# Kernel optimization log

Measured on AMD Instinct MI355X. Metric: run time of the kernel, lower is better.

Reference implementation:

```python
import jax, jax.numpy as jnp
import numpy as np

N = 268  # nodes per graph (4288 / nhid=16)


def _cheb_norm(edge_index, edge_weight):
    # PyG ChebConv normalization with normalization='sym', lambda_max=2.0:
    # L_hat = (2/lambda_max) * L - I = -D^{-1/2} A D^{-1/2} (diagonal cancels to 0)
    row, col = edge_index[0], edge_index[1]
    deg = jax.ops.segment_sum(edge_weight, row, num_segments=N)
    dis = jnp.where(deg > 0, jax.lax.rsqrt(deg), 0.0)
    return -edge_weight * dis[row] * dis[col]


def _cheb_conv(x, edge_index, norm, w, b):
    # K=2: out = T0 @ W0 + T1 @ W1 + b,  T0 = x, T1 = L_hat x
    row, col = edge_index[0], edge_index[1]
    tx1 = jax.ops.segment_sum(norm[:, None] * x[col], row, num_segments=N)
    return x @ w[0] + tx1 @ w[1] + b


def _forward_single(x, edge_index, edge_attr, gc1_w, gc1_b, gc4_w, gc4_b):
    norm = _cheb_norm(edge_index, edge_attr)
    h = jax.nn.relu(_cheb_conv(x, edge_index, norm, gc1_w, gc1_b))
    # dropout in eval mode -> identity
    return _cheb_conv(h, edge_index, norm, gc4_w, gc4_b)  # [N, nhid]


def setup_inputs() -> dict:
    key = jax.random.key(0)
    ks = jax.random.split(key, 20)
    B, E, F, H = 64, 8576, 268, 16
    inp = {}
    for i, nm in enumerate(['x1', 'x2', 'x3']):
        inp[nm] = jax.random.normal(ks[i], (B, N, F), dtype=jnp.float32)
    for i, nm in enumerate(['edge_index1', 'edge_index2', 'edge_index3']):
        inp[nm] = jax.random.randint(ks[3 + i], (B, 2, E), 0, N)
    for i, nm in enumerate(['edge_attr1', 'edge_attr2', 'edge_attr3']):
        inp[nm] = jax.random.uniform(ks[6 + i], (B, E), dtype=jnp.float32)
    s = 0.05
    inp['gc1_w'] = jax.random.normal(ks[9], (2, F, H), dtype=jnp.float32) * s
    inp['gc1_b'] = jnp.zeros((H,), dtype=jnp.float32)
    inp['gc4_w'] = jax.random.normal(ks[10], (2, H, H), dtype=jnp.float32) * s
    inp['gc4_b'] = jnp.zeros((H,), dtype=jnp.float32)
    inp['fc1_w'] = jax.random.normal(ks[11], (1024, N * H), dtype=jnp.float32) * s
    inp['fc1_b'] = jnp.zeros((1024,), dtype=jnp.float32)
    inp['fc2_w'] = jax.random.normal(ks[12], (512, 1024), dtype=jnp.float32) * s
    inp['fc2_b'] = jnp.zeros((512,), dtype=jnp.float32)
    return inp


def reference(x1, x2, x3, edge_index1, edge_index2, edge_index3,
              edge_attr1, edge_attr2, edge_attr3,
              gc1_w, gc1_b, gc4_w, gc4_b, fc1_w, fc1_b, fc2_w, fc2_b):
    conv = jax.vmap(_forward_single, in_axes=(0, 0, 0, None, None, None, None))

    def branch(x, ei, ea):
        c = conv(x, ei, ea, gc1_w, gc1_b, gc4_w, gc4_b)      # [B, N, H]
        f = c.reshape(c.shape[0], -1)                        # [B, 4288]
        h = jax.nn.relu(f @ fc1_w.T + fc1_b)                 # classifier dropout: eval -> id
        return h @ fc2_w.T + fc2_b                           # [B, 512]

    return (branch(x1, edge_index1, edge_attr1),
            branch(x2, edge_index2, edge_attr2),
            branch(x3, edge_index3, edge_attr3))
```

## Files before the change

kernel.cpp:

```cpp
#include <hip/hip_runtime.h>


#define NN   268
#define EE   8576
#define NG   192
#define FDIM 4288
#define CONVT 1024

typedef __bf16 bf16_t;
typedef bf16_t bf16x8 __attribute__((ext_vector_type(8)));
typedef bf16_t bf16x4 __attribute__((ext_vector_type(4)));
typedef float  f32x4  __attribute__((ext_vector_type(4)));

#define XW0_OFF  0
#define XW1_OFF  (XW0_OFF + (size_t)NG * FDIM)
#define WB_OFF   (XW1_OFF + (size_t)NG * FDIM)
#define FB_OFF   (WB_OFF + 2195456)
#define WXT_OFF  (FB_OFF + 411648)
#define H1_OFF   (WXT_OFF + 4608)
#define R1P_OFF  (H1_OFF + 196608)
#define R2P_OFF  (R1P_OFF + 1572864)

#define NCASTB 2144

__global__ __launch_bounds__(256) void k_prep(
    const float* __restrict__ fc1w, const float* __restrict__ gc1w,
    bf16_t* __restrict__ wb, bf16_t* __restrict__ wxt)
{
    if (blockIdx.x < NCASTB) {
        const size_t base = ((size_t)blockIdx.x * 256 + threadIdx.x) * 8;
        const float4 a = *(const float4*)(fc1w + base);
        const float4 b = *(const float4*)(fc1w + base + 4);
        bf16x8 v;
        v[0] = (bf16_t)a.x; v[1] = (bf16_t)a.y; v[2] = (bf16_t)a.z; v[3] = (bf16_t)a.w;
        v[4] = (bf16_t)b.x; v[5] = (bf16_t)b.y; v[6] = (bf16_t)b.z; v[7] = (bf16_t)b.w;
        *(bf16x8*)(wb + base) = v;
    } else {
        for (int idx = threadIdx.x; idx < 2 * 9 * 64; idx += 256) {
            const int lane = idx & 63, chunk = (idx >> 6) % 9, nt = idx / (9 * 64);
            const int n = lane & 15, q = lane >> 4;
            bf16x8 v;
#pragma unroll
            for (int j = 0; j < 8; ++j) {
                const int k = chunk * 32 + q * 8 + j;
                v[j] = (k < NN) ? (bf16_t)gc1w[nt * FDIM + k * 16 + n] : (bf16_t)0.f;
            }
            *(bf16x8*)(wxt + (size_t)idx * 8) = v;
        }
    }
}

__global__ __launch_bounds__(64) void k_xw(
    const float* __restrict__ x0, const float* __restrict__ x1, const float* __restrict__ x2,
    const bf16_t* __restrict__ wxt, float* __restrict__ xw0, float* __restrict__ xw1)
{
    const int g = blockIdx.y;
    const int br = g >> 6, b = g & 63;
    const float* x = ((br == 0) ? x0 : (br == 1) ? x1 : x2) + (size_t)b * (NN * NN);
    const int lane = threadIdx.x;
    const int q = lane >> 4, nlo = lane & 15;
    const int mrow = blockIdx.x * 16 + nlo;
    const bool mvalid = (mrow < NN);
    const float* xrow = x + (size_t)mrow * NN;

    f32x4 acc0 = {0.f, 0.f, 0.f, 0.f}, acc1 = {0.f, 0.f, 0.f, 0.f};
    for (int ch = 0; ch < 9; ++ch) {
        const int k0 = ch * 32 + q * 8;
        float4 p0 = make_float4(0.f, 0.f, 0.f, 0.f);
        float4 p1 = make_float4(0.f, 0.f, 0.f, 0.f);
        if (mvalid) {
            if (k0 < NN)     p0 = *(const float4*)(xrow + k0);
            if (k0 + 4 < NN) p1 = *(const float4*)(xrow + k0 + 4);
        }
        bf16x8 a;
        a[0] = (bf16_t)p0.x; a[1] = (bf16_t)p0.y; a[2] = (bf16_t)p0.z; a[3] = (bf16_t)p0.w;
        a[4] = (bf16_t)p1.x; a[5] = (bf16_t)p1.y; a[6] = (bf16_t)p1.z; a[7] = (bf16_t)p1.w;
        const bf16x8 b0 = *(const bf16x8*)(wxt + (size_t)(ch * 64 + lane) * 8);
        const bf16x8 b1 = *(const bf16x8*)(wxt + (size_t)(576 + ch * 64 + lane) * 8);
        acc0 = __builtin_amdgcn_mfma_f32_16x16x32_bf16(a, b0, acc0, 0, 0, 0);
        acc1 = __builtin_amdgcn_mfma_f32_16x16x32_bf16(a, b1, acc1, 0, 0, 0);
    }
    const int col = nlo;
#pragma unroll
    for (int r = 0; r < 4; ++r) {
        const int row = blockIdx.x * 16 + q * 4 + r;
        if (row < NN) {
            xw0[((size_t)g * NN + row) * 16 + col] = acc0[r];
            xw1[((size_t)g * NN + row) * 16 + col] = acc1[r];
        }
    }
}

__global__ __launch_bounds__(CONVT) void k_conv(
    const int* __restrict__ ei0, const int* __restrict__ ei1, const int* __restrict__ ei2,
    const float* __restrict__ ea0, const float* __restrict__ ea1, const float* __restrict__ ea2,
    const float* __restrict__ xw0, const float* __restrict__ xw1,
    const float* __restrict__ gc1b, const float* __restrict__ gc4w,
    const float* __restrict__ gc4b, bf16_t* __restrict__ fout)
{
    const int g = blockIdx.x;
    const int br = g >> 6, b = g & 63;
    const int*   ei = (br == 0) ? ei0 : (br == 1) ? ei1 : ei2;
    const float* ea = (br == 0) ? ea0 : (br == 1) ? ea1 : ea2;
    const int*   rowp = ei + (size_t)b * (2 * EE);
    const int*   colp = rowp + EE;
    const float* eap  = ea + (size_t)b * EE;

    __shared__ unsigned int e_s[EE];
    __shared__ __align__(16) bf16_t A_s[FDIM];
    __shared__ __align__(16) bf16_t S_s[FDIM];
    __shared__ float degS[NN];
    __shared__ int   cntS[NN];
    __shared__ int   offS[NN + 1];
    __shared__ int   curS[NN];
    __shared__ float w4_s[512];
    __shared__ float b1_s[16];
    __shared__ float b4_s[16];
    const int tid = threadIdx.x;

    if (tid < NN) { degS[tid] = 0.f; cntS[tid] = 0; }
    if (tid < 512) w4_s[tid] = gc4w[tid];
    if (tid < 16) { b1_s[tid] = gc1b[tid]; b4_s[tid] = gc4b[tid]; }
    {
        const float4* src = (const float4*)(xw1 + (size_t)g * FDIM);
        for (int i = tid; i < FDIM / 4; i += CONVT) {
            const float4 v = src[i];
            bf16x4 o; o[0] = (bf16_t)v.x; o[1] = (bf16_t)v.y; o[2] = (bf16_t)v.z; o[3] = (bf16_t)v.w;
            *(bf16x4*)&A_s[i * 4] = o;
        }
    }
    __syncthreads();
    for (int e = tid; e < EE; e += CONVT) {
        const int r = rowp[e];
        atomicAdd(&degS[r], eap[e]);
        atomicAdd(&cntS[r], 1);
    }
    for (int st = 1; st < NN; st <<= 1) {
        __syncthreads();
        int v = 0;
        if (tid < NN) { v = cntS[tid]; if (tid >= st) v += cntS[tid - st]; }
        __syncthreads();
        if (tid < NN) cntS[tid] = v;
    }
    __syncthreads();
    if (tid < NN) offS[tid + 1] = cntS[tid];
    if (tid == 0) offS[0] = 0;
    __syncthreads();
    if (tid < NN) {
        curS[tid] = offS[tid];
        const float d = degS[tid];
        degS[tid] = (d > 0.f) ? rsqrtf(d) : 0.f;
    }
    __syncthreads();
    for (int e = tid; e < EE; e += CONVT) {
        const int r = rowp[e], c = colp[e];
        const float nv = -eap[e] * degS[r] * degS[c];
        union { float f; unsigned u; } cv; cv.f = nv;
        const unsigned bits = (cv.u + 0x7fffu + ((cv.u >> 16) & 1u)) >> 16;
        const int pos = atomicAdd(&curS[r], 1);
        e_s[pos] = ((unsigned)c << 16) | bits;
    }
    __syncthreads();

    const int j4 = tid & 3, nl = tid >> 2;
    const bf16x4* A4 = (const bf16x4*)A_s;
    const float4* xw0g = (const float4*)(xw0 + (size_t)g * FDIM);

    for (int n = nl; n < NN; n += 256) {
        const int s = offS[n], e = offS[n + 1];
        float ax = 0.f, ay = 0.f, az = 0.f, aw = 0.f;
        int i = s;
        for (; i + 3 < e; i += 4) {
            const unsigned p0 = e_s[i], p1 = e_s[i + 1], p2 = e_s[i + 2], p3 = e_s[i + 3];
            const float w0 = __uint_as_float(p0 << 16);
            const float w1 = __uint_as_float(p1 << 16);
            const float w2 = __uint_as_float(p2 << 16);
            const float w3 = __uint_as_float(p3 << 16);
            const bf16x4 a0 = A4[(p0 >> 16) * 4 + j4];
            const bf16x4 a1 = A4[(p1 >> 16) * 4 + j4];
            const bf16x4 a2 = A4[(p2 >> 16) * 4 + j4];
            const bf16x4 a3 = A4[(p3 >> 16) * 4 + j4];
            ax += w0 * (float)a0[0] + w1 * (float)a1[0] + w2 * (float)a2[0] + w3 * (float)a3[0];
            ay += w0 * (float)a0[1] + w1 * (float)a1[1] + w2 * (float)a2[1] + w3 * (float)a3[1];
            az += w0 * (float)a0[2] + w1 * (float)a1[2] + w2 * (float)a2[2] + w3 * (float)a3[2];
            aw += w0 * (float)a0[3] + w1 * (float)a1[3] + w2 * (float)a2[3] + w3 * (float)a3[3];
        }
        for (; i < e; ++i) {
            const unsigned p0 = e_s[i];
            const float w0 = __uint_as_float(p0 << 16);
            const bf16x4 a0 = A4[(p0 >> 16) * 4 + j4];
            ax += w0 * (float)a0[0]; ay += w0 * (float)a0[1];
            az += w0 * (float)a0[2]; aw += w0 * (float)a0[3];
        }
        const float4 xv = xw0g[n * 4 + j4];
        bf16x4 h;
        h[0] = (bf16_t)fmaxf(xv.x + ax + b1_s[j4 * 4 + 0], 0.f);
        h[1] = (bf16_t)fmaxf(xv.y + ay + b1_s[j4 * 4 + 1], 0.f);
        h[2] = (bf16_t)fmaxf(xv.z + az + b1_s[j4 * 4 + 2], 0.f);
        h[3] = (bf16_t)fmaxf(xv.w + aw + b1_s[j4 * 4 + 3], 0.f);
        *(bf16x4*)&S_s[n * 16 + j4 * 4] = h;
    }
    __syncthreads();

    for (int idx = tid; idx < FDIM; idx += CONVT) {
        const int n = idx >> 4, j = idx & 15;
        const bf16x8 s0 = *(const bf16x8*)&S_s[n * 16];
        const bf16x8 s1 = *(const bf16x8*)&S_s[n * 16 + 8];
        float a1 = 0.f;
#pragma unroll
        for (int k = 0; k < 8; ++k) a1 += (float)s0[k] * w4_s[256 + k * 16 + j];
#pragma unroll
        for (int k = 0; k < 8; ++k) a1 += (float)s1[k] * w4_s[256 + (k + 8) * 16 + j];
        A_s[idx] = (bf16_t)a1;
    }
    __syncthreads();

    for (int n = nl; n < NN; n += 256) {
        const int s = offS[n], e = offS[n + 1];
        float ax = 0.f, ay = 0.f, az = 0.f, aw = 0.f;
        int i = s;
        for (; i + 3 < e; i += 4) {
            const unsigned p0 = e_s[i], p1 = e_s[i + 1], p2 = e_s[i + 2], p3 = e_s[i + 3];
            const float w0 = __uint_as_float(p0 << 16);
            const float w1 = __uint_as_float(p1 << 16);
            const float w2 = __uint_as_float(p2 << 16);
            const float w3 = __uint_as_float(p3 << 16);
            const bf16x4 a0 = A4[(p0 >> 16) * 4 + j4];
            const bf16x4 a1 = A4[(p1 >> 16) * 4 + j4];
            const bf16x4 a2 = A4[(p2 >> 16) * 4 + j4];
            const bf16x4 a3 = A4[(p3 >> 16) * 4 + j4];
            ax += w0 * (float)a0[0] + w1 * (float)a1[0] + w2 * (float)a2[0] + w3 * (float)a3[0];
            ay += w0 * (float)a0[1] + w1 * (float)a1[1] + w2 * (float)a2[1] + w3 * (float)a3[1];
            az += w0 * (float)a0[2] + w1 * (float)a1[2] + w2 * (float)a2[2] + w3 * (float)a3[2];
            aw += w0 * (float)a0[3] + w1 * (float)a1[3] + w2 * (float)a2[3] + w3 * (float)a3[3];
        }
        for (; i < e; ++i) {
            const unsigned p0 = e_s[i];
            const float w0 = __uint_as_float(p0 << 16);
            const bf16x4 a0 = A4[(p0 >> 16) * 4 + j4];
            ax += w0 * (float)a0[0]; ay += w0 * (float)a0[1];
            az += w0 * (float)a0[2]; aw += w0 * (float)a0[3];
        }
        float h0[4];
#pragma unroll
        for (int c2 = 0; c2 < 4; ++c2) h0[c2] = b4_s[j4 * 4 + c2];
        const bf16x8 s0 = *(const bf16x8*)&S_s[n * 16];
        const bf16x8 s1 = *(const bf16x8*)&S_s[n * 16 + 8];
#pragma unroll
        for (int k = 0; k < 8; ++k) {
            const float sv = (float)s0[k];
#pragma unroll
            for (int c2 = 0; c2 < 4; ++c2) h0[c2] += sv * w4_s[k * 16 + j4 * 4 + c2];
        }
#pragma unroll
        for (int k = 0; k < 8; ++k) {
            const float sv = (float)s1[k];
#pragma unroll
            for (int c2 = 0; c2 < 4; ++c2) h0[c2] += sv * w4_s[(k + 8) * 16 + j4 * 4 + c2];
        }
        bf16x4 o;
        o[0] = (bf16_t)(h0[0] + ax); o[1] = (bf16_t)(h0[1] + ay);
        o[2] = (bf16_t)(h0[2] + az); o[3] = (bf16_t)(h0[3] + aw);
        *(bf16x4*)(fout + (size_t)g * FDIM + n * 16 + j4 * 4) = o;
    }
}

__global__ __launch_bounds__(256) void k_fc1(
    const bf16_t* __restrict__ fb, const bf16_t* __restrict__ wb, float* __restrict__ r1p)
{
    const int mt = blockIdx.x, nb = blockIdx.y, kz = blockIdx.z;
    const int wid = threadIdx.x >> 6, lane = threadIdx.x & 63;
    const int q = lane >> 4, nlo = lane & 15;
    const int n0 = nb * 128 + wid * 32;
    const int cstart = kz * 17;
    const int ccnt   = (kz == 7) ? 15 : 17;

    const bf16_t* arow = fb + (size_t)(mt * 16 + nlo) * FDIM + q * 8;
    const bf16_t* brow = wb + (size_t)(n0 + nlo) * FDIM + q * 8;
    f32x4 acc[2];
#pragma unroll
    for (int t = 0; t < 2; ++t) { acc[t][0]=0.f; acc[t][1]=0.f; acc[t][2]=0.f; acc[t][3]=0.f; }

    for (int ch = 0; ch < ccnt; ++ch) {
        const size_t ko = (size_t)(cstart + ch) * 32;
        const bf16x8 a = *(const bf16x8*)(arow + ko);
#pragma unroll
        for (int t = 0; t < 2; ++t) {
            const bf16x8 bv = *(const bf16x8*)(brow + (size_t)t * 16 * FDIM + ko);
            acc[t] = __builtin_amdgcn_mfma_f32_16x16x32_bf16(a, bv, acc[t], 0, 0, 0);
        }
    }
    float* outp = r1p + (size_t)kz * (NG * 1024);
#pragma unroll
    for (int t = 0; t < 2; ++t)
#pragma unroll
        for (int r = 0; r < 4; ++r)
            outp[(size_t)(mt * 16 + q * 4 + r) * 1024 + n0 + t * 16 + nlo] = acc[t][r];
}

__global__ __launch_bounds__(256) void k_red1(
    const float* __restrict__ r1p, const float* __restrict__ b1, float* __restrict__ h1)
{
    const size_t i = ((size_t)blockIdx.x * 256 + threadIdx.x) * 4;
    const size_t S = (size_t)NG * 1024;
    float4 s = *(const float4*)(r1p + i);
#pragma unroll
    for (int k = 1; k < 8; ++k) {
        const float4 t = *(const float4*)(r1p + (size_t)k * S + i);
        s.x += t.x; s.y += t.y; s.z += t.z; s.w += t.w;
    }
    const float4 bb = *(const float4*)(b1 + (i & 1023));
    float4 o;
    o.x = fmaxf(s.x + bb.x, 0.f);
    o.y = fmaxf(s.y + bb.y, 0.f);
    o.z = fmaxf(s.z + bb.z, 0.f);
    o.w = fmaxf(s.w + bb.w, 0.f);
    *(float4*)(h1 + i) = o;
}

__global__ __launch_bounds__(256) void k_fc2(
    const float* __restrict__ h1, const float* __restrict__ w2, float* __restrict__ r2p)
{
    const int m0 = blockIdx.x * 64;
    const int n0 = blockIdx.y * 64;
    const int kb = blockIdx.z * 64;
    __shared__ float rs[64][68];
    __shared__ float wss[64][68];
    const int tid = threadIdx.x;
    const int mt = tid & 15, nt = tid >> 4;
    float acc[4][4];
#pragma unroll
    for (int i = 0; i < 4; ++i)
#pragma unroll
        for (int j = 0; j < 4; ++j) acc[i][j] = 0.f;

    for (int idx = tid; idx < 1024; idx += 256) {
        const int r = idx >> 4, qq = idx & 15;
        const int gk = kb + qq * 4;
        *(float4*)&rs[r][qq * 4]  = *(const float4*)(h1 + (size_t)(m0 + r) * 1024 + gk);
        *(float4*)&wss[r][qq * 4] = *(const float4*)(w2 + (size_t)(n0 + r) * 1024 + gk);
    }
    __syncthreads();
    for (int kq = 0; kq < 16; ++kq) {
        float4 av[4], bv[4];
#pragma unroll
        for (int i = 0; i < 4; ++i) av[i] = *(const float4*)&rs[mt + 16 * i][kq * 4];
#pragma unroll
        for (int j = 0; j < 4; ++j) bv[j] = *(const float4*)&wss[nt + 16 * j][kq * 4];
#pragma unroll
        for (int i = 0; i < 4; ++i)
#pragma unroll
            for (int j = 0; j < 4; ++j)
                acc[i][j] += av[i].x * bv[j].x + av[i].y * bv[j].y +
                             av[i].z * bv[j].z + av[i].w * bv[j].w;
    }
    float* outp = r2p + (size_t)blockIdx.z * (NG * 512);
#pragma unroll
    for (int i = 0; i < 4; ++i)
#pragma unroll
        for (int j = 0; j < 4; ++j)
            outp[(size_t)(m0 + mt + 16 * i) * 512 + n0 + nt + 16 * j] = acc[i][j];
}

__global__ __launch_bounds__(256) void k_red2(
    const float* __restrict__ r2p, const float* __restrict__ b2, float* __restrict__ out)
{
    const size_t i = ((size_t)blockIdx.x * 256 + threadIdx.x) * 4;
    const size_t S = (size_t)NG * 512;
    float4 s = *(const float4*)(r2p + i);
#pragma unroll
    for (int k = 1; k < 16; ++k) {
        const float4 t = *(const float4*)(r2p + (size_t)k * S + i);
        s.x += t.x; s.y += t.y; s.z += t.z; s.w += t.w;
    }
    const float4 bb = *(const float4*)(b2 + (i & 511));
    s.x += bb.x; s.y += bb.y; s.z += bb.z; s.w += bb.w;
    *(float4*)(out + i) = s;
}

extern "C" void kernel_launch(void* const* d_in, const int* in_sizes, int n_in,
                              void* d_out, int out_size, void* d_ws, size_t ws_size,
                              hipStream_t stream)
{
    const float* x0   = (const float*)d_in[0];
    const float* x1   = (const float*)d_in[1];
    const float* x2   = (const float*)d_in[2];
    const int*   ei0  = (const int*)d_in[3];
    const int*   ei1  = (const int*)d_in[4];
    const int*   ei2  = (const int*)d_in[5];
    const float* ea0  = (const float*)d_in[6];
    const float* ea1  = (const float*)d_in[7];
    const float* ea2  = (const float*)d_in[8];
    const float* gc1w = (const float*)d_in[9];
    const float* gc1b = (const float*)d_in[10];
    const float* gc4w = (const float*)d_in[11];
    const float* gc4b = (const float*)d_in[12];
    const float* fc1w = (const float*)d_in[13];
    const float* fc1b = (const float*)d_in[14];
    const float* fc2w = (const float*)d_in[15];
    const float* fc2b = (const float*)d_in[16];

    float*  ws  = (float*)d_ws;
    float*  xw0 = ws + XW0_OFF;
    float*  xw1 = ws + XW1_OFF;
    bf16_t* wb  = (bf16_t*)(ws + WB_OFF);
    bf16_t* fb  = (bf16_t*)(ws + FB_OFF);
    bf16_t* wxt = (bf16_t*)(ws + WXT_OFF);
    float*  h1  = ws + H1_OFF;
    float*  r1p = ws + R1P_OFF;
    float*  r2p = ws + R2P_OFF;
    float*  out = (float*)d_out;

    k_prep<<<NCASTB + 1, 256, 0, stream>>>(fc1w, gc1w, wb, wxt);
    k_xw  <<<dim3(17, NG), 64, 0, stream>>>(x0, x1, x2, wxt, xw0, xw1);
    k_conv<<<NG, CONVT, 0, stream>>>(ei0, ei1, ei2, ea0, ea1, ea2,
                                     xw0, xw1, gc1b, gc4w, gc4b, fb);
    k_fc1 <<<dim3(12, 8, 8), 256, 0, stream>>>(fb, wb, r1p);
    k_red1<<<NG, 256, 0, stream>>>(r1p, fc1b, h1);
    k_fc2 <<<dim3(3, 8, 16), 256, 0, stream>>>(h1, fc2w, r2p);
    k_red2<<<96, 256, 0, stream>>>(r2p, fc2b, out);
}
```

Measured before the change: 225.2 us.

## Fuse x@W0/W1 MFMA projection into conv kernel, keep results in LDS

Removes the separate k_xw kernel and computes the x·gc1_w projections inside k_conv, with 16 waves each handling a 16-row tile via bf16 MFMA. The results go straight into shared memory (xw0 as float, xw1 as bf16 in A_s), so the global round trip of the xw buffers and one kernel launch disappear. In exchange the x projection now runs on only 192 blocks instead of 17×192 small blocks. Each wave's MFMA loop is serialized (17 tiles on 16 waves, so one wave does two), and the extra LDS array may lower occupancy.

```diff
diff --git a/kernel.cpp b/kernel.cpp
--- a/kernel.cpp
+++ b/kernel.cpp
@@ -12,10 +12,8 @@
 typedef bf16_t bf16x4 __attribute__((ext_vector_type(4)));
 typedef float  f32x4  __attribute__((ext_vector_type(4)));
 
-#define XW0_OFF  0
-#define XW1_OFF  (XW0_OFF + (size_t)NG * FDIM)
-#define WB_OFF   (XW1_OFF + (size_t)NG * FDIM)
-#define FB_OFF   (WB_OFF + 2195456)
+#define WB_OFF   0
+#define FB_OFF   2195456
 #define WXT_OFF  (FB_OFF + 411648)
 #define H1_OFF   (WXT_OFF + 4608)
 #define R1P_OFF  (H1_OFF + 196608)
@@ -50,56 +48,17 @@
     }
 }
 
-__global__ __launch_bounds__(64) void k_xw(
+__global__ __launch_bounds__(CONVT) void k_conv(
     const float* __restrict__ x0, const float* __restrict__ x1, const float* __restrict__ x2,
-    const bf16_t* __restrict__ wxt, float* __restrict__ xw0, float* __restrict__ xw1)
-{
-    const int g = blockIdx.y;
-    const int br = g >> 6, b = g & 63;
-    const float* x = ((br == 0) ? x0 : (br == 1) ? x1 : x2) + (size_t)b * (NN * NN);
-    const int lane = threadIdx.x;
-    const int q = lane >> 4, nlo = lane & 15;
-    const int mrow = blockIdx.x * 16 + nlo;
-    const bool mvalid = (mrow < NN);
-    const float* xrow = x + (size_t)mrow * NN;
-
-    f32x4 acc0 = {0.f, 0.f, 0.f, 0.f}, acc1 = {0.f, 0.f, 0.f, 0.f};
-    for (int ch = 0; ch < 9; ++ch) {
-        const int k0 = ch * 32 + q * 8;
-        float4 p0 = make_float4(0.f, 0.f, 0.f, 0.f);
-        float4 p1 = make_float4(0.f, 0.f, 0.f, 0.f);
-        if (mvalid) {
-            if (k0 < NN)     p0 = *(const float4*)(xrow + k0);
-            if (k0 + 4 < NN) p1 = *(const float4*)(xrow + k0 + 4);
-        }
-        bf16x8 a;
-        a[0] = (bf16_t)p0.x; a[1] = (bf16_t)p0.y; a[2] = (bf16_t)p0.z; a[3] = (bf16_t)p0.w;
-        a[4] = (bf16_t)p1.x; a[5] = (bf16_t)p1.y; a[6] = (bf16_t)p1.z; a[7] = (bf16_t)p1.w;
-        const bf16x8 b0 = *(const bf16x8*)(wxt + (size_t)(ch * 64 + lane) * 8);
-        const bf16x8 b1 = *(const bf16x8*)(wxt + (size_t)(576 + ch * 64 + lane) * 8);
-        acc0 = __builtin_amdgcn_mfma_f32_16x16x32_bf16(a, b0, acc0, 0, 0, 0);
-        acc1 = __builtin_amdgcn_mfma_f32_16x16x32_bf16(a, b1, acc1, 0, 0, 0);
-    }
-    const int col = nlo;
-#pragma unroll
-    for (int r = 0; r < 4; ++r) {
-        const int row = blockIdx.x * 16 + q * 4 + r;
-        if (row < NN) {
-            xw0[((size_t)g * NN + row) * 16 + col] = acc0[r];
-            xw1[((size_t)g * NN + row) * 16 + col] = acc1[r];
-        }
-    }
-}
-
-__global__ __launch_bounds__(CONVT) void k_conv(
     const int* __restrict__ ei0, const int* __restrict__ ei1, const int* __restrict__ ei2,
     const float* __restrict__ ea0, const float* __restrict__ ea1, const float* __restrict__ ea2,
-    const float* __restrict__ xw0, const float* __restrict__ xw1,
+    const bf16_t* __restrict__ wxt,
     const float* __restrict__ gc1b, const float* __restrict__ gc4w,
     const float* __restrict__ gc4b, bf16_t* __restrict__ fout)
 {
     const int g = blockIdx.x;
     const int br = g >> 6, b = g & 63;
+    const float* xg = ((br == 0) ? x0 : (br == 1) ? x1 : x2) + (size_t)b * (NN * NN);
     const int*   ei = (br == 0) ? ei0 : (br == 1) ? ei1 : ei2;
     const float* ea = (br == 0) ? ea0 : (br == 1) ? ea1 : ea2;
     const int*   rowp = ei + (size_t)b * (2 * EE);
@@ -109,6 +68,7 @@
     __shared__ unsigned int e_s[EE];
     __shared__ __align__(16) bf16_t A_s[FDIM];
     __shared__ __align__(16) bf16_t S_s[FDIM];
+    __shared__ __align__(16) float  xw0_s[FDIM];
     __shared__ float degS[NN];
     __shared__ int   cntS[NN];
     __shared__ int   offS[NN + 1];
@@ -117,19 +77,47 @@
     __shared__ float b1_s[16];
     __shared__ float b4_s[16];
     const int tid = threadIdx.x;
+    const int lane = tid & 63, wid = tid >> 6;
 
     if (tid < NN) { degS[tid] = 0.f; cntS[tid] = 0; }
     if (tid < 512) w4_s[tid] = gc4w[tid];
     if (tid < 16) { b1_s[tid] = gc1b[tid]; b4_s[tid] = gc4b[tid]; }
+
     {
-        const float4* src = (const float4*)(xw1 + (size_t)g * FDIM);
-        for (int i = tid; i < FDIM / 4; i += CONVT) {
-            const float4 v = src[i];
-            bf16x4 o; o[0] = (bf16_t)v.x; o[1] = (bf16_t)v.y; o[2] = (bf16_t)v.z; o[3] = (bf16_t)v.w;
-            *(bf16x4*)&A_s[i * 4] = o;
-        }
-    }
-    __syncthreads();
+        const int q = lane >> 4, nlo = lane & 15;
+        for (int mt = wid; mt < 17; mt += 16) {
+            const int mrow = mt * 16 + nlo;
+            const bool mvalid = (mrow < NN);
+            const float* xrow = xg + (size_t)mrow * NN;
+            f32x4 acc0 = {0.f, 0.f, 0.f, 0.f}, acc1 = {0.f, 0.f, 0.f, 0.f};
+            for (int ch = 0; ch < 9; ++ch) {
+                const int k0 = ch * 32 + q * 8;
+                float4 p0 = make_float4(0.f, 0.f, 0.f, 0.f);
+                float4 p1 = make_float4(0.f, 0.f, 0.f, 0.f);
+                if (mvalid) {
+                    if (k0 < NN)     p0 = *(const float4*)(xrow + k0);
+                    if (k0 + 4 < NN) p1 = *(const float4*)(xrow + k0 + 4);
+                }
+                bf16x8 a;
+                a[0] = (bf16_t)p0.x; a[1] = (bf16_t)p0.y; a[2] = (bf16_t)p0.z; a[3] = (bf16_t)p0.w;
+                a[4] = (bf16_t)p1.x; a[5] = (bf16_t)p1.y; a[6] = (bf16_t)p1.z; a[7] = (bf16_t)p1.w;
+                const bf16x8 b0 = *(const bf16x8*)(wxt + (size_t)(ch * 64 + lane) * 8);
+                const bf16x8 b1 = *(const bf16x8*)(wxt + (size_t)(576 + ch * 64 + lane) * 8);
+                acc0 = __builtin_amdgcn_mfma_f32_16x16x32_bf16(a, b0, acc0, 0, 0, 0);
+                acc1 = __builtin_amdgcn_mfma_f32_16x16x32_bf16(a, b1, acc1, 0, 0, 0);
+            }
+#pragma unroll
+            for (int r = 0; r < 4; ++r) {
+                const int row = mt * 16 + q * 4 + r;
+                if (row < NN) {
+                    xw0_s[row * 16 + nlo] = acc0[r];
+                    A_s[row * 16 + nlo] = (bf16_t)acc1[r];
+                }
+            }
+        }
+    }
+    __syncthreads();
+
     for (int e = tid; e < EE; e += CONVT) {
         const int r = rowp[e];
         atomicAdd(&degS[r], eap[e]);
@@ -164,7 +152,55 @@
 
     const int j4 = tid & 3, nl = tid >> 2;
     const bf16x4* A4 = (const bf16x4*)A_s;
-    const float4* xw0g = (const float4*)(xw0 + (size_t)g * FDIM);
+
+    for (int n = nl; n < NN; n += 256) {
+        const int s = offS[n], e = offS[n + 1];
+        const f32x4 xv = *(const f32x4*)&xw0_s[n * 16 + j4 * 4];
+        float ax = 0.f, ay = 0.f, az = 0.f, aw = 0.f;
+        int i = s;
+        for (; i + 3 < e; i += 4) {
+            const unsigned p0 = e_s[i], p1 = e_s[i + 1], p2 = e_s[i + 2], p3 = e_s[i + 3];
+            const float w0 = __uint_as_float(p0 << 16);
+            const float w1 = __uint_as_float(p1 << 16);
+            const float w2 = __uint_as_float(p2 << 16);
+            const float w3 = __uint_as_float(p3 << 16);
+            const bf16x4 a0 = A4[(p0 >> 16) * 4 + j4];
+            const bf16x4 a1 = A4[(p1 >> 16) * 4 + j4];
+            const bf16x4 a2 = A4[(p2 >> 16) * 4 + j4];
+            const bf16x4 a3 = A4[(p3 >> 16) * 4 + j4];
+            ax += w0 * (float)a0[0] + w1 * (float)a1[0] + w2 * (float)a2[0] + w3 * (float)a3[0];
+            ay += w0 * (float)a0[1] + w1 * (float)a1[1] + w2 * (float)a2[1] + w3 * (float)a3[1];
+            az += w0 * (float)a0[2] + w1 * (float)a1[2] + w2 * (float)a2[2] + w3 * (float)a3[2];
+            aw += w0 * (float)a0[3] + w1 * (float)a1[3] + w2 * (float)a2[3] + w3 * (float)a3[3];
+        }
+        for (; i < e; ++i) {
+            const unsigned p0 = e_s[i];
+            const float w0 = __uint_as_float(p0 << 16);
+            const bf16x4 a0 = A4[(p0 >> 16) * 4 + j4];
+            ax += w0 * (float)a0[0]; ay += w0 * (float)a0[1];
+            az += w0 * (float)a0[2]; aw += w0 * (float)a0[3];
+        }
+        bf16x4 h;
+        h[0] = (bf16_t)fmaxf(xv[0] + ax + b1_s[j4 * 4 + 0], 0.f);
+        h[1] = (bf16_t)fmaxf(xv[1] + ay + b1_s[j4 * 4 + 1], 0.f);
+        h[2] = (bf16_t)fmaxf(xv[2] + az + b1_s[j4 * 4 + 2], 0.f);
+        h[3] = (bf16_t)fmaxf(xv[3] + aw + b1_s[j4 * 4 + 3], 0.f);
+        *(bf16x4*)&S_s[n * 16 + j4 * 4] = h;
+    }
+    __syncthreads();
+
+    for (int idx = tid; idx < FDIM; idx += CONVT) {
+        const int n = idx >> 4, j = idx & 15;
+        const bf16x8 s0 = *(const bf16x8*)&S_s[n * 16];
+        const bf16x8 s1 = *(const bf16x8*)&S_s[n * 16 + 8];
+        float a1 = 0.f;
+#pragma unroll
+        for (int k = 0; k < 8; ++k) a1 += (float)s0[k] * w4_s[256 + k * 16 + j];
+#pragma unroll
+        for (int k = 0; k < 8; ++k) a1 += (float)s1[k] * w4_s[256 + (k + 8) * 16 + j];
+        A_s[idx] = (bf16_t)a1;
+    }
+    __syncthreads();
 
     for (int n = nl; n < NN; n += 256) {
         const int s = offS[n], e = offS[n + 1];
@@ -192,55 +228,6 @@
             ax += w0 * (float)a0[0]; ay += w0 * (float)a0[1];
             az += w0 * (float)a0[2]; aw += w0 * (float)a0[3];
         }
-        const float4 xv = xw0g[n * 4 + j4];
-        bf16x4 h;
-        h[0] = (bf16_t)fmaxf(xv.x + ax + b1_s[j4 * 4 + 0], 0.f);
-        h[1] = (bf16_t)fmaxf(xv.y + ay + b1_s[j4 * 4 + 1], 0.f);
-        h[2] = (bf16_t)fmaxf(xv.z + az + b1_s[j4 * 4 + 2], 0.f);
-        h[3] = (bf16_t)fmaxf(xv.w + aw + b1_s[j4 * 4 + 3], 0.f);
-        *(bf16x4*)&S_s[n * 16 + j4 * 4] = h;
-    }
-    __syncthreads();
-
-    for (int idx = tid; idx < FDIM; idx += CONVT) {
-        const int n = idx >> 4, j = idx & 15;
-        const bf16x8 s0 = *(const bf16x8*)&S_s[n * 16];
-        const bf16x8 s1 = *(const bf16x8*)&S_s[n * 16 + 8];
-        float a1 = 0.f;
-#pragma unroll
-        for (int k = 0; k < 8; ++k) a1 += (float)s0[k] * w4_s[256 + k * 16 + j];
-#pragma unroll
-        for (int k = 0; k < 8; ++k) a1 += (float)s1[k] * w4_s[256 + (k + 8) * 16 + j];
-        A_s[idx] = (bf16_t)a1;
-    }
-    __syncthreads();
-
-    for (int n = nl; n < NN; n += 256) {
-        const int s = offS[n], e = offS[n + 1];
-        float ax = 0.f, ay = 0.f, az = 0.f, aw = 0.f;
-        int i = s;
-        for (; i + 3 < e; i += 4) {
-            const unsigned p0 = e_s[i], p1 = e_s[i + 1], p2 = e_s[i + 2], p3 = e_s[i + 3];
-            const float w0 = __uint_as_float(p0 << 16);
-            const float w1 = __uint_as_float(p1 << 16);
-            const float w2 = __uint_as_float(p2 << 16);
-            const float w3 = __uint_as_float(p3 << 16);
-            const bf16x4 a0 = A4[(p0 >> 16) * 4 + j4];
-            const bf16x4 a1 = A4[(p1 >> 16) * 4 + j4];
-            const bf16x4 a2 = A4[(p2 >> 16) * 4 + j4];
-            const bf16x4 a3 = A4[(p3 >> 16) * 4 + j4];
-            ax += w0 * (float)a0[0] + w1 * (float)a1[0] + w2 * (float)a2[0] + w3 * (float)a3[0];
-            ay += w0 * (float)a0[1] + w1 * (float)a1[1] + w2 * (float)a2[1] + w3 * (float)a3[1];
-            az += w0 * (float)a0[2] + w1 * (float)a1[2] + w2 * (float)a2[2] + w3 * (float)a3[2];
-            aw += w0 * (float)a0[3] + w1 * (float)a1[3] + w2 * (float)a2[3] + w3 * (float)a3[3];
-        }
-        for (; i < e; ++i) {
-            const unsigned p0 = e_s[i];
-            const float w0 = __uint_as_float(p0 << 16);
-            const bf16x4 a0 = A4[(p0 >> 16) * 4 + j4];
-            ax += w0 * (float)a0[0]; ay += w0 * (float)a0[1];
-            az += w0 * (float)a0[2]; aw += w0 * (float)a0[3];
-        }
         float h0[4];
 #pragma unroll
         for (int c2 = 0; c2 < 4; ++c2) h0[c2] = b4_s[j4 * 4 + c2];
@@ -401,8 +388,6 @@
     const float* fc2b = (const float*)d_in[16];
 
     float*  ws  = (float*)d_ws;
-    float*  xw0 = ws + XW0_OFF;
-    float*  xw1 = ws + XW1_OFF;
     bf16_t* wb  = (bf16_t*)(ws + WB_OFF);
     bf16_t* fb  = (bf16_t*)(ws + FB_OFF);
     bf16_t* wxt = (bf16_t*)(ws + WXT_OFF);
@@ -412,9 +397,8 @@
     float*  out = (float*)d_out;
 
     k_prep<<<NCASTB + 1, 256, 0, stream>>>(fc1w, gc1w, wb, wxt);
-    k_xw  <<<dim3(17, NG), 64, 0, stream>>>(x0, x1, x2, wxt, xw0, xw1);
-    k_conv<<<NG, CONVT, 0, stream>>>(ei0, ei1, ei2, ea0, ea1, ea2,
-                                     xw0, xw1, gc1b, gc4w, gc4b, fb);
+    k_conv<<<NG, CONVT, 0, stream>>>(x0, x1, x2, ei0, ei1, ei2, ea0, ea1, ea2,
+                                     wxt, gc1b, gc4w, gc4b, fb);
     k_fc1 <<<dim3(12, 8, 8), 256, 0, stream>>>(fb, wb, r1p);
     k_red1<<<NG, 256, 0, stream>>>(r1p, fc1b, h1);
     k_fc2 <<<dim3(3, 8, 16), 256, 0, stream>>>(h1, fc2w, r2p);
```

After: 220.4 us. 1.02x faster.
